# Performance work log

Hardware: AMD Instinct MI355X
Metric: run time of the kernel (lower is better)

## Reference

```python
import jax, jax.numpy as jnp
import numpy as np

N, E = 20000, 100000
D_IN, H1, C1 = 512, 8, 64   # conv1: 512 -> 8 heads x 64, concat -> 512
H2, C2 = 4, 128             # conv2: 512 -> 4 heads x 128, mean -> 128


def setup_inputs() -> dict:
    key = jax.random.key(0)
    k = jax.random.split(key, 12)
    s_in = 1.0 / np.sqrt(D_IN).astype(np.float32)
    return {
        "street_embedding": jax.random.normal(k[0], (N, D_IN), jnp.float32),
        "edge_index": jax.random.randint(k[1], (2, E), 0, N),
        "y": jax.random.randint(k[2], (N,), 0, C2),
        "train_mask": jax.random.bernoulli(k[3], 0.5, (N,)),
        "W1": jax.random.normal(k[4], (D_IN, H1 * C1), jnp.float32) * s_in,
        "att_src1": jax.random.normal(k[5], (H1, C1), jnp.float32) * 0.1,
        "att_dst1": jax.random.normal(k[6], (H1, C1), jnp.float32) * 0.1,
        "b1": jnp.zeros((H1 * C1,), jnp.float32),
        "W2": jax.random.normal(k[7], (H1 * C1, H2 * C2), jnp.float32) * s_in,
        "att_src2": jax.random.normal(k[8], (H2, C2), jnp.float32) * 0.1,
        "att_dst2": jax.random.normal(k[9], (H2, C2), jnp.float32) * 0.1,
        "b2": jnp.zeros((C2,), jnp.float32),
    }


def _gat_conv(x, W, a_src, a_dst, b, src, dst, n, H, C, concat):
    # linear transform (no bias, as in PyG GATConv's internal lin)
    xp = (x @ W).reshape(n, H, C)                      # [N,H,C]
    asrc = jnp.einsum('nhc,hc->nh', xp, a_src)         # [N,H]
    adst = jnp.einsum('nhc,hc->nh', xp, a_dst)
    e = jax.nn.leaky_relu(asrc[src] + adst[dst], 0.2)  # [E',H] edge scores
    # softmax over incoming edges per destination node
    m = jax.lax.stop_gradient(jax.ops.segment_max(e, dst, num_segments=n))
    ex = jnp.exp(e - m[dst])
    denom = jax.ops.segment_sum(ex, dst, num_segments=n)
    alpha = ex / (denom[dst] + 1e-16)                  # [E',H]
    out = jax.ops.segment_sum(alpha[:, :, None] * xp[src], dst, num_segments=n)  # [N,H,C]
    if concat:
        return out.reshape(n, H * C) + b
    return out.mean(axis=1) + b


def reference(street_embedding, edge_index, y, train_mask,
              W1, att_src1, att_dst1, b1, W2, att_src2, att_dst2, b2):
    n = street_embedding.shape[0]
    loop = jnp.arange(n)
    # PyG GATConv adds self-loops by default
    src = jnp.concatenate([edge_index[0], loop])
    dst = jnp.concatenate([edge_index[1], loop])
    # dropout layers are identity in eval mode
    h = _gat_conv(street_embedding, W1, att_src1, att_dst1, b1, src, dst, n, H1, C1, True)
    h = jax.nn.elu(h)
    out = _gat_conv(h, W2, att_src2, att_dst2, b2, src, dst, n, H2, C2, False)  # [N,C2]
    # CrossEntropyLoss, mean over train_mask nodes (weighted mean, jit-safe)
    logp = jax.nn.log_softmax(out, axis=-1)
    ce = -jnp.take_along_axis(logp, y[:, None], axis=-1)[:, 0]
    w = train_mask.astype(out.dtype)
    loss_su = jnp.sum(w * ce) / jnp.sum(w)
    return (loss_su, out)
```

## Files before the change

kernel.cpp:

```cpp
#include <hip/hip_runtime.h>
#include <cmath>

#define D_IN 512
#define HC   512
#define NH1  8
#define NC1  64
#define NH2  4
#define NC2  128
#define BM 128
#define BN 128
#define BK 64

typedef __attribute__((ext_vector_type(8))) short short8;
typedef __attribute__((ext_vector_type(4))) float f32x4;

__device__ inline ushort f2bf(float f) {
  unsigned u = __float_as_uint(f);
  return (ushort)((u + 0x7FFFu + ((u >> 16) & 1u)) >> 16);
}
__device__ inline float bf2f(ushort b) { return __uint_as_float(((unsigned)b) << 16); }

__global__ void k_cast_all(const float* __restrict__ x, ushort* __restrict__ Abf,
                           const float* __restrict__ W1, const float* __restrict__ W2,
                           ushort* __restrict__ Wt1, ushort* __restrict__ Wt2, int n4x) {
  const int KN = D_IN * HC;
  int i = blockIdx.x * blockDim.x + threadIdx.x;
  if (i < n4x) {
    float4 v = ((const float4*)x)[i];
    ushort4 r = { f2bf(v.x), f2bf(v.y), f2bf(v.z), f2bf(v.w) };
    ((ushort4*)Abf)[i] = r;
  } else {
    int idx = i - n4x;
    if (idx >= 2 * KN) return;
    const float* W = (idx < KN) ? W1 : W2;
    ushort* Wt = (idx < KN) ? Wt1 : Wt2;
    int j = (idx < KN) ? idx : idx - KN;
    int n = j / D_IN, k = j - n * D_IN;
    Wt[j] = f2bf(W[(size_t)k * HC + n]);
  }
}

template<int H>
__global__ void k_gemm_bf16(const ushort* __restrict__ A, const ushort* __restrict__ Bt,
                            ushort* __restrict__ Cbf,
                            const float* __restrict__ att_s, const float* __restrict__ att_d,
                            float* __restrict__ asrc, float* __restrict__ adst, int M) {
  constexpr int C = HC / H;
  __shared__ __align__(16) ushort As[BM * BK];
  __shared__ __align__(16) ushort Bs[BN * BK];
  int t = threadIdx.x;
  int m0 = blockIdx.y * BM;
  int n0 = blockIdx.x * BN;
  int wave = t >> 6, lane = t & 63;
  int ln = lane & 15, qd = lane >> 4;
  int wm = (wave >> 1) * 64, wn = (wave & 1) * 64;

  f32x4 acc[4][4] = {};

  int g = t >> 6, ct = (t >> 4) & 3, lt = t & 15;
  int rA0 = m0 + g * 16 + lt;      if (rA0 > M - 1) rA0 = M - 1;
  int rA1 = m0 + 64 + g * 16 + lt; if (rA1 > M - 1) rA1 = M - 1;
  const ushort* gA0 = A + (size_t)rA0 * D_IN + ct * 8;
  const ushort* gA1 = A + (size_t)rA1 * D_IN + ct * 8;
  const ushort* gB0 = Bt + (size_t)(n0 + g * 16 + lt) * D_IN + ct * 8;
  const ushort* gB1 = Bt + (size_t)(n0 + 64 + g * 16 + lt) * D_IN + ct * 8;

  for (int k0 = 0; k0 < D_IN; k0 += BK) {
    __syncthreads();
#pragma unroll
    for (int h = 0; h < 2; ++h) {
      int ko = k0 + h * 32;
      int lo = h * 4096;
      __builtin_amdgcn_global_load_lds(
          (const __attribute__((address_space(1))) void*)(gA0 + ko),
          (__attribute__((address_space(3))) void*)(As + lo + t * 8), 16, 0, 0);
      __builtin_amdgcn_global_load_lds(
          (const __attribute__((address_space(1))) void*)(gA1 + ko),
          (__attribute__((address_space(3))) void*)(As + lo + 2048 + t * 8), 16, 0, 0);
      __builtin_amdgcn_global_load_lds(
          (const __attribute__((address_space(1))) void*)(gB0 + ko),
          (__attribute__((address_space(3))) void*)(Bs + lo + t * 8), 16, 0, 0);
      __builtin_amdgcn_global_load_lds(
          (const __attribute__((address_space(1))) void*)(gB1 + ko),
          (__attribute__((address_space(3))) void*)(Bs + lo + 2048 + t * 8), 16, 0, 0);
    }
    __syncthreads();
#pragma unroll
    for (int h = 0; h < 2; ++h) {
      int lo = h * 4096;
      short8 a[4], bb[4];
#pragma unroll
      for (int i = 0; i < 4; ++i)
        a[i] = *(const short8*)&As[lo + (((wave >> 1) * 4 + i) * 4 + qd) * 128 + ln * 8];
#pragma unroll
      for (int j = 0; j < 4; ++j)
        bb[j] = *(const short8*)&Bs[lo + (((wave & 1) * 4 + j) * 4 + qd) * 128 + ln * 8];
#pragma unroll
      for (int i = 0; i < 4; ++i)
#pragma unroll
        for (int j = 0; j < 4; ++j)
          acc[i][j] = __builtin_amdgcn_mfma_f32_16x16x32_bf16(a[i], bb[j], acc[i][j], 0, 0, 0);
    }
  }

#pragma unroll
  for (int i = 0; i < 4; ++i) {
#pragma unroll
    for (int reg = 0; reg < 4; ++reg) {
      int row = m0 + wm + i * 16 + qd * 4 + reg;
      if (row >= M) continue;
#pragma unroll
      for (int j = 0; j < 4; ++j)
        Cbf[(size_t)row * HC + n0 + wn + j * 16 + ln] = f2bf(acc[i][j][reg]);
    }
  }

  int colbase = n0 + wn;
  int h = colbase / C;
  float sa[4], da[4];
#pragma unroll
  for (int j = 0; j < 4; ++j) {
    int c = (colbase % C) + j * 16 + ln;
    sa[j] = att_s[h * C + c];
    da[j] = att_d[h * C + c];
  }
#pragma unroll
  for (int i = 0; i < 4; ++i) {
#pragma unroll
    for (int reg = 0; reg < 4; ++reg) {
      float ps = acc[i][0][reg] * sa[0] + acc[i][1][reg] * sa[1]
               + acc[i][2][reg] * sa[2] + acc[i][3][reg] * sa[3];
      float pd = acc[i][0][reg] * da[0] + acc[i][1][reg] * da[1]
               + acc[i][2][reg] * da[2] + acc[i][3][reg] * da[3];
#pragma unroll
      for (int o = 1; o < 16; o <<= 1) { ps += __shfl_xor(ps, o); pd += __shfl_xor(pd, o); }
      int row = m0 + wm + i * 16 + qd * 4 + reg;
      if (ln == 0 && row < M) {
        if (C == 64) {
          asrc[row * H + h] = ps; adst[row * H + h] = pd;
        } else {
          int sub = (colbase >> 6) & 1;
          asrc[(row * H + h) * 2 + sub] = ps;
          adst[(row * H + h) * 2 + sub] = pd;
        }
      }
    }
  }
}

__global__ void k_hist(const int* __restrict__ ei, int E, int Etot, int* __restrict__ cnt) {
  int e = blockIdx.x * blockDim.x + threadIdx.x;
  if (e >= Etot) return;
  int d = (e < E) ? ei[E + e] : e - E;
  atomicAdd(&cnt[d], 1);
}

__global__ void k_scan(const int* __restrict__ cnt, int* __restrict__ rowstart, int N) {
  int tid = threadIdx.x;
  int T = (N + 1023) / 1024;
  int base = tid * T;
  int sum = 0;
  for (int i = 0; i < T; ++i) { int j = base + i; if (j < N) sum += cnt[j]; }
  int lane = tid & 63, w = tid >> 6;
  int v = sum;
#pragma unroll
  for (int off = 1; off < 64; off <<= 1) {
    int u = __shfl_up(v, off);
    if (lane >= off) v += u;
  }
  __shared__ int wsum[16];
  if (lane == 63) wsum[w] = v;
  __syncthreads();
  if (tid < 16) {
    int tv = wsum[tid];
#pragma unroll
    for (int off = 1; off < 16; off <<= 1) {
      int u = __shfl_up(tv, off);
      if (tid >= off) tv += u;
    }
    wsum[tid] = tv;
  }
  __syncthreads();
  int wave_prefix = (w == 0) ? 0 : wsum[w - 1];
  int run = wave_prefix + v - sum;
  for (int i = 0; i < T; ++i) {
    int j = base + i;
    if (j < N) { rowstart[j] = run; run += cnt[j]; }
  }
  if (tid == 1023) rowstart[N] = run;
}

__global__ void k_scatter(const int* __restrict__ ei, int E, int Etot,
                          const int* __restrict__ rowstart, int* __restrict__ cursor,
                          int* __restrict__ csr_src) {
  int e = blockIdx.x * blockDim.x + threadIdx.x;
  if (e >= Etot) return;
  int s = (e < E) ? ei[e] : e - E;
  int d = (e < E) ? ei[E + e] : e - E;
  int pos = atomicAdd(&cursor[d], 1);
  csr_src[rowstart[d] + pos] = s;
}

template<int H, int MODE>
__global__ __launch_bounds__(256)
void k_agg(const int* __restrict__ rowstart, const int* __restrict__ csr_src,
           const float* __restrict__ asrc, const float* __restrict__ adst,
           const ushort* __restrict__ xp, ushort* __restrict__ hout,
           float* __restrict__ out2, const float* __restrict__ bias,
           const int* __restrict__ y, const int* __restrict__ msk,
           float* __restrict__ acc2, int N) {
  constexpr int C = HC / H;
  int wave = threadIdx.x >> 6, lane = threadIdx.x & 63;
  int n = blockIdx.x * 4 + wave;
  if (n >= N) return;
  int h = (lane * 8) / C;

  float adn = (MODE == 1) ? adst[n * H + h]
                          : adst[(n * H + h) * 2] + adst[(n * H + h) * 2 + 1];
  float acc[8] = {};
  float wsum = 0.f;
  int beg = rowstart[n], end = rowstart[n + 1];

#define SCORE(s) ((MODE == 1) ? asrc[(s) * H + h] \
                              : asrc[((s) * H + h) * 2] + asrc[((s) * H + h) * 2 + 1])

  int i = beg;
  for (; i + 1 < end; i += 2) {
    int s0 = csr_src[i], s1 = csr_src[i + 1];
    float v0 = SCORE(s0) + adn;
    float v1 = SCORE(s1) + adn;
    short8 r0 = ((const short8*)xp)[(size_t)s0 * 64 + lane];
    short8 r1 = ((const short8*)xp)[(size_t)s1 * 64 + lane];
    v0 = (v0 > 0.f) ? v0 : 0.2f * v0;
    v1 = (v1 > 0.f) ? v1 : 0.2f * v1;
    float w0 = __expf(v0), w1 = __expf(v1);
#pragma unroll
    for (int k = 0; k < 8; ++k)
      acc[k] += w0 * bf2f((ushort)r0[k]) + w1 * bf2f((ushort)r1[k]);
    wsum += w0 + w1;
  }
  if (i < end) {
    int s0 = csr_src[i];
    float v0 = SCORE(s0) + adn;
    short8 r0 = ((const short8*)xp)[(size_t)s0 * 64 + lane];
    v0 = (v0 > 0.f) ? v0 : 0.2f * v0;
    float w0 = __expf(v0);
#pragma unroll
    for (int k = 0; k < 8; ++k) acc[k] += w0 * bf2f((ushort)r0[k]);
    wsum += w0;
  }
#undef SCORE

  float rdn = 1.0f / (wsum + 1e-16f);
#pragma unroll
  for (int k = 0; k < 8; ++k) acc[k] *= rdn;

  if (MODE == 1) {
    short8 rr;
#pragma unroll
    for (int k = 0; k < 8; ++k) {
      float v = acc[k] + bias[lane * 8 + k];
      v = (v > 0.f) ? v : expm1f(v);
      rr[k] = (short)f2bf(v);
    }
    ((short8*)hout)[(size_t)n * 64 + lane] = rr;
  } else {
    float lg[8];
#pragma unroll
    for (int k = 0; k < 8; ++k) {
      float v = acc[k];
      v += __shfl_xor(v, 16);
      v += __shfl_xor(v, 32);
      lg[k] = v * 0.25f + bias[(lane & 15) * 8 + k];
    }
    if (lane < 16) {
#pragma unroll
      for (int k = 0; k < 8; ++k)
        out2[(size_t)n * NC2 + lane * 8 + k] = lg[k];
    }
    float mx = lg[0];
#pragma unroll
    for (int k = 1; k < 8; ++k) mx = fmaxf(mx, lg[k]);
#pragma unroll
    for (int o = 1; o < 16; o <<= 1) mx = fmaxf(mx, __shfl_xor(mx, o));
    float se = 0.f;
#pragma unroll
    for (int k = 0; k < 8; ++k) se += __expf(lg[k] - mx);
#pragma unroll
    for (int o = 1; o < 16; o <<= 1) se += __shfl_xor(se, o);
    int ty = y[n];
    float myv = lg[0];
#pragma unroll
    for (int k = 1; k < 8; ++k) myv = ((ty & 7) == k) ? lg[k] : myv;
    float tlg = __shfl(myv, ty >> 3);
    if (lane == 0 && msk[n] != 0) {
      float ce = mx + logf(se) - tlg;
      int slot = n & 127;
      atomicAdd(&acc2[slot], ce);
      atomicAdd(&acc2[128 + slot], 1.0f);
    }
  }
}

__global__ void k_final(const float* __restrict__ acc2, float* __restrict__ out0) {
  int tid = threadIdx.x;
  float ce = acc2[tid], ct = acc2[128 + tid];
#pragma unroll
  for (int o = 32; o > 0; o >>= 1) { ce += __shfl_xor(ce, o); ct += __shfl_xor(ct, o); }
  __shared__ float s[4];
  if ((tid & 63) == 0) { s[(tid >> 6) * 2] = ce; s[(tid >> 6) * 2 + 1] = ct; }
  __syncthreads();
  if (tid == 0) out0[0] = (s[0] + s[2]) / (s[1] + s[3]);
}

extern "C" void kernel_launch(void* const* d_in, const int* in_sizes, int n_in,
                              void* d_out, int out_size, void* d_ws, size_t ws_size,
                              hipStream_t stream) {
  const float* x   = (const float*)d_in[0];
  const int*   ei  = (const int*)d_in[1];
  const int*   y   = (const int*)d_in[2];
  const int*   msk = (const int*)d_in[3];
  const float* W1  = (const float*)d_in[4];
  const float* as1 = (const float*)d_in[5];
  const float* ad1 = (const float*)d_in[6];
  const float* b1  = (const float*)d_in[7];
  const float* W2  = (const float*)d_in[8];
  const float* as2 = (const float*)d_in[9];
  const float* ad2 = (const float*)d_in[10];
  const float* b2  = (const float*)d_in[11];
  float* out = (float*)d_out;

  int N = in_sizes[0] / D_IN;
  int E = in_sizes[1] / 2;
  int Etot = E + N;

  float* ws = (float*)d_ws;
  size_t NF = (size_t)N * HC;
  float* asr1 = ws;
  float* adt1 = asr1 + (size_t)N * NH1;
  float* asr2 = adt1 + (size_t)N * NH1;
  float* adt2 = asr2 + (size_t)N * 2 * NH2;
  float* acc2 = adt2 + (size_t)N * 2 * NH2;
  int*   cnt    = (int*)(acc2 + 256);
  int*   cursor = cnt + N;
  size_t zero_bytes = (256 + 2 * (size_t)N) * sizeof(float);
  int*   rowstart = cursor + N;
  int*   csr_src  = rowstart + N + 1;
  ushort* xpbf = (ushort*)((((uintptr_t)(csr_src + Etot)) + 15) & ~(uintptr_t)15);
  ushort* Abf = xpbf + NF;
  ushort* Wt1 = Abf + NF;
  ushort* Wt2 = Wt1 + (size_t)D_IN * HC;

  hipMemsetAsync(acc2, 0, zero_bytes, stream);

  int n4x = (int)(NF / 4);
  int cast_total = n4x + 2 * D_IN * HC;
  k_cast_all<<<(cast_total + 255) / 256, 256, 0, stream>>>(x, Abf, W1, W2, Wt1, Wt2, n4x);

  k_hist<<<(Etot + 255) / 256, 256, 0, stream>>>(ei, E, Etot, cnt);
  k_scan<<<1, 1024, 0, stream>>>(cnt, rowstart, N);
  k_scatter<<<(Etot + 255) / 256, 256, 0, stream>>>(ei, E, Etot, rowstart, cursor, csr_src);

  dim3 ggrid(HC / BN, (N + BM - 1) / BM);
  int agrid = (N + 3) / 4;

  k_gemm_bf16<NH1><<<ggrid, 256, 0, stream>>>(Abf, Wt1, xpbf, as1, ad1, asr1, adt1, N);
  k_agg<NH1, 1><<<agrid, 256, 0, stream>>>(rowstart, csr_src, asr1, adt1, xpbf, Abf,
                                           nullptr, b1, nullptr, nullptr, nullptr, N);

  k_gemm_bf16<NH2><<<ggrid, 256, 0, stream>>>(Abf, Wt2, xpbf, as2, ad2, asr2, adt2, N);
  k_agg<NH2, 2><<<agrid, 256, 0, stream>>>(rowstart, csr_src, asr2, adt2, xpbf, nullptr,
                                           out + 1, b2, y, msk, acc2, N);

  k_final<<<1, 128, 0, stream>>>(acc2, out);
}
```

Before: 300.8 us.

## Retile GEMM to full-width 64-row blocks and fuse per-head attention reductions

The GEMM now gives each block 64 rows and all 512 output columns with a K-step of 32, so every wave owns whole heads. The attention-score dot products can then be reduced inside the kernel without split partial sums. This removes the two-part asrc/adst layout for layer 2 and the extra loads and adds in the aggregation kernel. The cost is a larger B tile reloaded per block, more accumulator registers per wave (4x8 MFMA tiles), and more K iterations with more barriers.

New measurement: 369.0 us. +22.7%, slower.

```diff
diff --git a/kernel.cpp b/kernel.cpp
--- a/kernel.cpp
+++ b/kernel.cpp
@@ -7,9 +7,8 @@
 #define NC1  64
 #define NH2  4
 #define NC2  128
-#define BM 128
-#define BN 128
-#define BK 64
+#define GBM 64
+#define GBK 32
 
 typedef __attribute__((ext_vector_type(8))) short short8;
 typedef __attribute__((ext_vector_type(4))) float f32x4;
@@ -41,107 +40,97 @@
 }
 
 template<int H>
-__global__ void k_gemm_bf16(const ushort* __restrict__ A, const ushort* __restrict__ Bt,
-                            ushort* __restrict__ Cbf,
-                            const float* __restrict__ att_s, const float* __restrict__ att_d,
-                            float* __restrict__ asrc, float* __restrict__ adst, int M) {
+__global__ __launch_bounds__(256)
+void k_gemm_bf16(const ushort* __restrict__ A, const ushort* __restrict__ Bt,
+                 ushort* __restrict__ Cbf,
+                 const float* __restrict__ att_s, const float* __restrict__ att_d,
+                 float* __restrict__ asrc, float* __restrict__ adst, int M) {
   constexpr int C = HC / H;
-  __shared__ __align__(16) ushort As[BM * BK];
-  __shared__ __align__(16) ushort Bs[BN * BK];
+  constexpr int HG = 128 / C;
+  constexpr int JPH = 8 / HG;
+  __shared__ __align__(16) ushort As[GBM * GBK];
+  __shared__ __align__(16) ushort Bs[512 * GBK];
   int t = threadIdx.x;
-  int m0 = blockIdx.y * BM;
-  int n0 = blockIdx.x * BN;
+  int m0 = blockIdx.x * GBM;
   int wave = t >> 6, lane = t & 63;
   int ln = lane & 15, qd = lane >> 4;
-  int wm = (wave >> 1) * 64, wn = (wave & 1) * 64;
-
-  f32x4 acc[4][4] = {};
+
+  f32x4 acc[4][8] = {};
 
   int g = t >> 6, ct = (t >> 4) & 3, lt = t & 15;
-  int rA0 = m0 + g * 16 + lt;      if (rA0 > M - 1) rA0 = M - 1;
-  int rA1 = m0 + 64 + g * 16 + lt; if (rA1 > M - 1) rA1 = M - 1;
-  const ushort* gA0 = A + (size_t)rA0 * D_IN + ct * 8;
-  const ushort* gA1 = A + (size_t)rA1 * D_IN + ct * 8;
-  const ushort* gB0 = Bt + (size_t)(n0 + g * 16 + lt) * D_IN + ct * 8;
-  const ushort* gB1 = Bt + (size_t)(n0 + 64 + g * 16 + lt) * D_IN + ct * 8;
-
-  for (int k0 = 0; k0 < D_IN; k0 += BK) {
+  int rA = m0 + g * 16 + lt; if (rA > M - 1) rA = M - 1;
+  const ushort* gA = A + (size_t)rA * D_IN + ct * 8;
+  const ushort* gB = Bt + (size_t)(g * 16 + lt) * D_IN + ct * 8;
+
+  for (int k0 = 0; k0 < D_IN; k0 += GBK) {
     __syncthreads();
-#pragma unroll
-    for (int h = 0; h < 2; ++h) {
-      int ko = k0 + h * 32;
-      int lo = h * 4096;
+    __builtin_amdgcn_global_load_lds(
+        (const __attribute__((address_space(1))) void*)(gA + k0),
+        (__attribute__((address_space(3))) void*)(As + t * 8), 16, 0, 0);
+#pragma unroll
+    for (int r = 0; r < 8; ++r)
       __builtin_amdgcn_global_load_lds(
-          (const __attribute__((address_space(1))) void*)(gA0 + ko),
-          (__attribute__((address_space(3))) void*)(As + lo + t * 8), 16, 0, 0);
-      __builtin_amdgcn_global_load_lds(
-          (const __attribute__((address_space(1))) void*)(gA1 + ko),
-          (__attribute__((address_space(3))) void*)(As + lo + 2048 + t * 8), 16, 0, 0);
-      __builtin_amdgcn_global_load_lds(
-          (const __attribute__((address_space(1))) void*)(gB0 + ko),
-          (__attribute__((address_space(3))) void*)(Bs + lo + t * 8), 16, 0, 0);
-      __builtin_amdgcn_global_load_lds(
-          (const __attribute__((address_space(1))) void*)(gB1 + ko),
-          (__attribute__((address_space(3))) void*)(Bs + lo + 2048 + t * 8), 16, 0, 0);
-    }
+          (const __attribute__((address_space(1))) void*)(gB + (size_t)r * 64 * D_IN + k0),
+          (__attribute__((address_space(3))) void*)(Bs + r * 2048 + t * 8), 16, 0, 0);
     __syncthreads();
-#pragma unroll
-    for (int h = 0; h < 2; ++h) {
-      int lo = h * 4096;
-      short8 a[4], bb[4];
-#pragma unroll
-      for (int i = 0; i < 4; ++i)
-        a[i] = *(const short8*)&As[lo + (((wave >> 1) * 4 + i) * 4 + qd) * 128 + ln * 8];
-#pragma unroll
-      for (int j = 0; j < 4; ++j)
-        bb[j] = *(const short8*)&Bs[lo + (((wave & 1) * 4 + j) * 4 + qd) * 128 + ln * 8];
-#pragma unroll
-      for (int i = 0; i < 4; ++i)
-#pragma unroll
-        for (int j = 0; j < 4; ++j)
-          acc[i][j] = __builtin_amdgcn_mfma_f32_16x16x32_bf16(a[i], bb[j], acc[i][j], 0, 0, 0);
-    }
+    short8 a[4], bb[8];
+#pragma unroll
+    for (int i = 0; i < 4; ++i)
+      a[i] = *(const short8*)&As[(i * 4 + qd) * 128 + ln * 8];
+#pragma unroll
+    for (int j = 0; j < 8; ++j) {
+      int col = wave * 128 + j * 16;
+      int region = col >> 6;
+      int rg = (col & 63) >> 4;
+      bb[j] = *(const short8*)&Bs[region * 2048 + (rg * 4 + qd) * 128 + ln * 8];
+    }
+#pragma unroll
+    for (int i = 0; i < 4; ++i)
+#pragma unroll
+      for (int j = 0; j < 8; ++j)
+        acc[i][j] = __builtin_amdgcn_mfma_f32_16x16x32_bf16(a[i], bb[j], acc[i][j], 0, 0, 0);
   }
 
 #pragma unroll
   for (int i = 0; i < 4; ++i) {
 #pragma unroll
     for (int reg = 0; reg < 4; ++reg) {
-      int row = m0 + wm + i * 16 + qd * 4 + reg;
+      int row = m0 + i * 16 + qd * 4 + reg;
       if (row >= M) continue;
 #pragma unroll
-      for (int j = 0; j < 4; ++j)
-        Cbf[(size_t)row * HC + n0 + wn + j * 16 + ln] = f2bf(acc[i][j][reg]);
-    }
-  }
-
-  int colbase = n0 + wn;
-  int h = colbase / C;
-  float sa[4], da[4];
-#pragma unroll
-  for (int j = 0; j < 4; ++j) {
-    int c = (colbase % C) + j * 16 + ln;
+      for (int j = 0; j < 8; ++j)
+        Cbf[(size_t)row * HC + wave * 128 + j * 16 + ln] = f2bf(acc[i][j][reg]);
+    }
+  }
+
+  float sa[8], da[8];
+#pragma unroll
+  for (int j = 0; j < 8; ++j) {
+    int h = wave * HG + j / JPH;
+    int c = (j % JPH) * 16 + ln;
     sa[j] = att_s[h * C + c];
     da[j] = att_d[h * C + c];
   }
 #pragma unroll
-  for (int i = 0; i < 4; ++i) {
-#pragma unroll
-    for (int reg = 0; reg < 4; ++reg) {
-      float ps = acc[i][0][reg] * sa[0] + acc[i][1][reg] * sa[1]
-               + acc[i][2][reg] * sa[2] + acc[i][3][reg] * sa[3];
-      float pd = acc[i][0][reg] * da[0] + acc[i][1][reg] * da[1]
-               + acc[i][2][reg] * da[2] + acc[i][3][reg] * da[3];
-#pragma unroll
-      for (int o = 1; o < 16; o <<= 1) { ps += __shfl_xor(ps, o); pd += __shfl_xor(pd, o); }
-      int row = m0 + wm + i * 16 + qd * 4 + reg;
-      if (ln == 0 && row < M) {
-        if (C == 64) {
-          asrc[row * H + h] = ps; adst[row * H + h] = pd;
-        } else {
-          int sub = (colbase >> 6) & 1;
-          asrc[(row * H + h) * 2 + sub] = ps;
-          adst[(row * H + h) * 2 + sub] = pd;
+  for (int hg = 0; hg < HG; ++hg) {
+    int h = wave * HG + hg;
+#pragma unroll
+    for (int i = 0; i < 4; ++i) {
+#pragma unroll
+      for (int reg = 0; reg < 4; ++reg) {
+        float ps = 0.f, pd = 0.f;
+#pragma unroll
+        for (int jj = 0; jj < JPH; ++jj) {
+          int j = hg * JPH + jj;
+          ps += acc[i][j][reg] * sa[j];
+          pd += acc[i][j][reg] * da[j];
+        }
+#pragma unroll
+        for (int o = 1; o < 16; o <<= 1) { ps += __shfl_xor(ps, o); pd += __shfl_xor(pd, o); }
+        int row = m0 + i * 16 + qd * 4 + reg;
+        if (ln == 0 && row < M) {
+          asrc[row * H + h] = ps;
+          adst[row * H + h] = pd;
         }
       }
     }
@@ -215,20 +204,16 @@
   if (n >= N) return;
   int h = (lane * 8) / C;
 
-  float adn = (MODE == 1) ? adst[n * H + h]
-                          : adst[(n * H + h) * 2] + adst[(n * H + h) * 2 + 1];
+  float adn = adst[n * H + h];
   float acc[8] = {};
   float wsum = 0.f;
   int beg = rowstart[n], end = rowstart[n + 1];
 
-#define SCORE(s) ((MODE == 1) ? asrc[(s) * H + h] \
-                              : asrc[((s) * H + h) * 2] + asrc[((s) * H + h) * 2 + 1])
-
   int i = beg;
   for (; i + 1 < end; i += 2) {
     int s0 = csr_src[i], s1 = csr_src[i + 1];
-    float v0 = SCORE(s0) + adn;
-    float v1 = SCORE(s1) + adn;
+    float v0 = asrc[s0 * H + h] + adn;
+    float v1 = asrc[s1 * H + h] + adn;
     short8 r0 = ((const short8*)xp)[(size_t)s0 * 64 + lane];
     short8 r1 = ((const short8*)xp)[(size_t)s1 * 64 + lane];
     v0 = (v0 > 0.f) ? v0 : 0.2f * v0;
@@ -241,7 +226,7 @@
   }
   if (i < end) {
     int s0 = csr_src[i];
-    float v0 = SCORE(s0) + adn;
+    float v0 = asrc[s0 * H + h] + adn;
     short8 r0 = ((const short8*)xp)[(size_t)s0 * 64 + lane];
     v0 = (v0 > 0.f) ? v0 : 0.2f * v0;
     float w0 = __expf(v0);
@@ -249,7 +234,6 @@
     for (int k = 0; k < 8; ++k) acc[k] += w0 * bf2f((ushort)r0[k]);
     wsum += w0;
   }
-#undef SCORE
 
   float rdn = 1.0f / (wsum + 1e-16f);
 #pragma unroll
@@ -339,8 +323,8 @@
   float* asr1 = ws;
   float* adt1 = asr1 + (size_t)N * NH1;
   float* asr2 = adt1 + (size_t)N * NH1;
-  float* adt2 = asr2 + (size_t)N * 2 * NH2;
-  float* acc2 = adt2 + (size_t)N * 2 * NH2;
+  float* adt2 = asr2 + (size_t)N * NH2;
+  float* acc2 = adt2 + (size_t)N * NH2;
   int*   cnt    = (int*)(acc2 + 256);
   int*   cursor = cnt + N;
   size_t zero_bytes = (256 + 2 * (size_t)N) * sizeof(float);
@@ -361,7 +345,7 @@
   k_scan<<<1, 1024, 0, stream>>>(cnt, rowstart, N);
   k_scatter<<<(Etot + 255) / 256, 256, 0, stream>>>(ei, E, Etot, rowstart, cursor, csr_src);
 
-  dim3 ggrid(HC / BN, (N + BM - 1) / BM);
+  int ggrid = (N + GBM - 1) / GBM;
   int agrid = (N + 3) / 4;
 
   k_gemm_bf16<NH1><<<ggrid, 256, 0, stream>>>(Abf, Wt1, xpbf, as1, ad1, asr1, adt1, N);
```
